# Optimization experiments

Hardware: AMD Instinct MI355X
Metric: run time of the kernel (lower is better)

The kernel has to match this reference:

```python
import jax, jax.numpy as jnp
import numpy as np

N = 50000       # num_nodes
E = 1_600_000   # num_edges (avg degree 32)
F_IN, HID, F_OUT = 128, 128, 64


def setup_inputs() -> dict:
    key = jax.random.key(0)
    k0, k1, k2, k3 = jax.random.split(key, 4)
    x = jax.random.normal(k0, (1, N, F_IN), dtype=jnp.float32)
    edge_index = jax.random.randint(k1, (2, E), 0, N, dtype=jnp.int32)
    # GCNConv weights (glorot-ish scale) and zero biases
    W1 = jax.random.normal(k2, (F_IN, HID), dtype=jnp.float32) / np.float32(np.sqrt(F_IN))
    b1 = jnp.zeros((HID,), dtype=jnp.float32)
    W2 = jax.random.normal(k3, (HID, F_OUT), dtype=jnp.float32) / np.float32(np.sqrt(HID))
    b2 = jnp.zeros((F_OUT,), dtype=jnp.float32)
    return {"x": x, "edge_index": edge_index, "W1": W1, "b1": b1, "W2": W2, "b2": b2}


def _gcn_layer(h, src, dst, norm, W, b, n):
    # linear transform then symmetric-normalized scatter-add aggregation
    h = h @ W                              # [N, F_out]
    msg = h[src] * norm[:, None]           # [E+N, F_out] gathered messages
    agg = jax.ops.segment_sum(msg, dst, num_segments=n)
    return agg + b


def reference(x, edge_index, W1, b1, W2, b2):
    xn = x[0]                              # [N, F_in] node feature matrix
    n = xn.shape[0]
    src, dst = edge_index[0], edge_index[1]
    # add self-loops (GCNConv default)
    loops = jnp.arange(n, dtype=src.dtype)
    src = jnp.concatenate([src, loops])
    dst = jnp.concatenate([dst, loops])
    # symmetric normalization: deg^-1/2[src] * deg^-1/2[dst] (deg >= 1 w/ self-loops)
    deg = jax.ops.segment_sum(jnp.ones(dst.shape, dtype=xn.dtype), dst, num_segments=n)
    dinv = jax.lax.rsqrt(deg)
    norm = dinv[src] * dinv[dst]
    h = jax.nn.relu(_gcn_layer(xn, src, dst, norm, W1, b1, n))
    out = jax.nn.relu(_gcn_layer(h, src, dst, norm, W2, b2, n))
    return out
```

## Files before the change

### kernel.cpp

```cpp
#include <hip/hip_runtime.h>
#include <hip/hip_fp16.h>


#define TILE 8192
#define BIN_CAP 2560

typedef _Float16 half8 __attribute__((ext_vector_type(8)));
typedef float floatx4 __attribute__((ext_vector_type(4)));

__global__ __launch_bounds__(256) void bin_kernel(const int* __restrict__ src,
                                                  const int* __restrict__ dst, int E,
                                                  int nbins,
                                                  int* __restrict__ binCnt,
                                                  unsigned* __restrict__ recs) {
    extern __shared__ int lds[];
    int* cnt = lds;
    int* gbase = lds + nbins;
    int tid = threadIdx.x;
    for (int i = tid; i < nbins; i += 256) cnt[i] = 0;
    __syncthreads();

    int t0 = blockIdx.x * TILE;
    int tEnd = min(t0 + TILE, E);

    for (int e = t0 + tid; e < tEnd; e += 256)
        atomicAdd(&cnt[dst[e] >> 6], 1);
    __syncthreads();

    for (int i = tid; i < nbins; i += 256) {
        int c = cnt[i];
        gbase[i] = (c > 0) ? atomicAdd(&binCnt[i], c) : 0;
        cnt[i] = 0;
    }
    __syncthreads();

    for (int e = t0 + tid; e < tEnd; e += 256) {
        int d = dst[e];
        int s = src[e];
        int b = d >> 6;
        int r = atomicAdd(&cnt[b], 1);
        int g = gbase[b] + r;
        if (g < BIN_CAP)
            recs[(size_t)b * BIN_CAP + g] = ((unsigned)(d & 63) << 16) | (unsigned)s;
    }
}

__global__ __launch_bounds__(256) void sort_bins(const unsigned* __restrict__ recs,
                                                 const int* __restrict__ binCnt,
                                                 unsigned short* __restrict__ sortedG,
                                                 int* __restrict__ startG,
                                                 float* __restrict__ dinv, int N) {
    __shared__ unsigned short sorted[BIN_CAP];
    __shared__ int c64[64];
    __shared__ int start[65];
    __shared__ int cursor[64];
    int b = blockIdx.x, tid = threadIdx.x;
    int lane = tid & 63, wave = tid >> 6;

    if (tid < 64) c64[tid] = 0;
    __syncthreads();
    int cnt = min(binCnt[b], BIN_CAP);
    const unsigned* bin = recs + (size_t)b * BIN_CAP;

    for (int i = tid; i < cnt; i += 256)
        atomicAdd(&c64[bin[i] >> 16], 1);
    __syncthreads();

    if (wave == 0) {
        int c = c64[lane];
        int v = c;
        #pragma unroll
        for (int off = 1; off < 64; off <<= 1) {
            int t = __shfl_up(v, off);
            if (lane >= off) v += t;
        }
        start[lane] = v - c;
        cursor[lane] = v - c;
        startG[b * 65 + lane] = v - c;
        if (lane == 63) { start[64] = v; startG[b * 65 + 64] = v; }
        int n = (b << 6) + lane;
        if (n < N) dinv[n] = rsqrtf((float)(c + 1));
    }
    __syncthreads();

    for (int i = tid; i < cnt; i += 256) {
        unsigned r = bin[i];
        int pos = atomicAdd(&cursor[r >> 16], 1);
        sorted[pos] = (unsigned short)(r & 0xFFFFu);
    }
    __syncthreads();
    unsigned short* sg = sortedG + (size_t)b * BIN_CAP;
    for (int i = tid; i < cnt; i += 256) sg[i] = sorted[i];
}

template <int COLS, bool FP32IN>
__global__ __launch_bounds__(256) void gemm_mfma(const void* __restrict__ Xv,
                                                 const float* __restrict__ W,
                                                 const float* __restrict__ dinv,
                                                 __half* __restrict__ Y, int N) {
    constexpr int LDA = 136;
    __shared__ __align__(16) _Float16 aT[64 * LDA];
    __shared__ __align__(16) _Float16 bT[COLS * LDA];

    int tid = threadIdx.x;
    int lane = tid & 63, wave = tid >> 6;
    int row0 = blockIdx.x * 64;

    for (int i = tid * 4; i < 64 * 128; i += 1024) {
        int r = i >> 7, k = i & 127;
        int gr = row0 + r;
        if (FP32IN) {
            float4 v = make_float4(0.f, 0.f, 0.f, 0.f);
            if (gr < N) v = *(const float4*)&((const float*)Xv)[(size_t)gr * 128 + k];
            __half2 p0 = __floats2half2_rn(v.x, v.y);
            __half2 p1 = __floats2half2_rn(v.z, v.w);
            *(uint2*)&aT[r * LDA + k] = make_uint2(*(uint*)&p0, *(uint*)&p1);
        } else {
            ushort4 u = make_ushort4(0, 0, 0, 0);
            if (gr < N) u = *(const ushort4*)&((const __half*)Xv)[(size_t)gr * 128 + k];
            *(ushort4*)&aT[r * LDA + k] = u;
        }
    }
    for (int i = tid; i < 128 * COLS; i += 256) {
        int k = i / COLS, n = i % COLS;
        bT[n * LDA + k] = (_Float16)W[i];
    }
    __syncthreads();

    constexpr int NT = COLS / 16;
    floatx4 acc[NT];
    #pragma unroll
    for (int t = 0; t < NT; t++) acc[t] = (floatx4){0.f, 0.f, 0.f, 0.f};

    int m = lane & 15, q = lane >> 4;
    const _Float16* arow = &aT[(wave * 16 + m) * LDA + q * 8];

    #pragma unroll
    for (int ks = 0; ks < 4; ks++) {
        half8 af = *(const half8*)&arow[ks * 32];
        #pragma unroll
        for (int t = 0; t < NT; t++) {
            half8 bf = *(const half8*)&bT[(t * 16 + m) * LDA + ks * 32 + q * 8];
            acc[t] = __builtin_amdgcn_mfma_f32_16x16x32_f16(af, bf, acc[t], 0, 0, 0);
        }
    }
    __syncthreads();

    float dv[4];
    #pragma unroll
    for (int r = 0; r < 4; r++) {
        int gr = row0 + wave * 16 + q * 4 + r;
        dv[r] = (gr < N) ? dinv[gr] : 0.0f;
    }
    #pragma unroll
    for (int t = 0; t < NT; t++)
        #pragma unroll
        for (int r = 0; r < 4; r++)
            aT[(wave * 16 + q * 4 + r) * LDA + t * 16 + m] = (_Float16)(dv[r] * acc[t][r]);
    __syncthreads();

    for (int i = tid; i < 64 * (COLS / 2); i += 256) {
        int r = i / (COLS / 2), c = i % (COLS / 2);
        int gr = row0 + r;
        if (gr < N)
            ((uint*)Y)[(size_t)gr * (COLS / 2) + c] = *(uint*)&aT[r * LDA + c * 2];
    }
}

__global__ __launch_bounds__(512) void agg_128(const __half* __restrict__ G,
                                               const unsigned short* __restrict__ sortedG,
                                               const int* __restrict__ startG,
                                               const float* __restrict__ dinv,
                                               const float* __restrict__ bias,
                                               __half* __restrict__ out, int N) {
    __shared__ unsigned short buf[BIN_CAP];
    __shared__ int st[33];
    int b = blockIdx.x, half_ = blockIdx.y;
    int tid = threadIdx.x, lane = tid & 63, wave = tid >> 6;
    int r0 = half_ * 32;

    if (tid < 33) st[tid] = startG[b * 65 + r0 + tid];
    __syncthreads();
    int S0 = st[0], S1 = st[32];
    const unsigned short* sg = sortedG + (size_t)b * BIN_CAP;
    for (int i = tid; i < S1 - S0; i += 512) buf[i] = sg[S0 + i];
    __syncthreads();

    float bx = bias[lane * 2], by = bias[lane * 2 + 1];
    for (int rr = 0; rr < 4; rr++) {
        int row = wave * 4 + rr;
        int n = (b << 6) + r0 + row;
        if (n >= N) continue;
        int jst = st[row] - S0, jen = st[row + 1] - S0;
        float2 self = __half22float2(*(const __half2*)&G[(size_t)n * 128 + lane * 2]);
        float ax = self.x, ay = self.y;
        int j = jst;
        for (; j + 8 <= jen; j += 8) {
            int s0 = buf[j],     s1 = buf[j + 1];
            int s2 = buf[j + 2], s3 = buf[j + 3];
            int s4 = buf[j + 4], s5 = buf[j + 5];
            int s6 = buf[j + 6], s7 = buf[j + 7];
            float2 v0 = __half22float2(*(const __half2*)&G[(size_t)s0 * 128 + lane * 2]);
            float2 v1 = __half22float2(*(const __half2*)&G[(size_t)s1 * 128 + lane * 2]);
            float2 v2 = __half22float2(*(const __half2*)&G[(size_t)s2 * 128 + lane * 2]);
            float2 v3 = __half22float2(*(const __half2*)&G[(size_t)s3 * 128 + lane * 2]);
            float2 v4 = __half22float2(*(const __half2*)&G[(size_t)s4 * 128 + lane * 2]);
            float2 v5 = __half22float2(*(const __half2*)&G[(size_t)s5 * 128 + lane * 2]);
            float2 v6 = __half22float2(*(const __half2*)&G[(size_t)s6 * 128 + lane * 2]);
            float2 v7 = __half22float2(*(const __half2*)&G[(size_t)s7 * 128 + lane * 2]);
            ax += ((v0.x + v1.x) + (v2.x + v3.x)) + ((v4.x + v5.x) + (v6.x + v7.x));
            ay += ((v0.y + v1.y) + (v2.y + v3.y)) + ((v4.y + v5.y) + (v6.y + v7.y));
        }
        for (; j < jen; j++) {
            int s = buf[j];
            float2 v = __half22float2(*(const __half2*)&G[(size_t)s * 128 + lane * 2]);
            ax += v.x; ay += v.y;
        }
        float di = dinv[n];
        float ox = fmaxf(fmaf(di, ax, bx), 0.0f);
        float oy = fmaxf(fmaf(di, ay, by), 0.0f);
        *(__half2*)&out[(size_t)n * 128 + lane * 2] = __floats2half2_rn(ox, oy);
    }
}

__global__ __launch_bounds__(512) void agg_64(const __half* __restrict__ G,
                                              const unsigned short* __restrict__ sortedG,
                                              const int* __restrict__ startG,
                                              const float* __restrict__ dinv,
                                              const float* __restrict__ bias,
                                              float* __restrict__ out, int N) {
    __shared__ unsigned short buf[BIN_CAP];
    __shared__ int st[33];
    int b = blockIdx.x, half_ = blockIdx.y;
    int tid = threadIdx.x, lane = tid & 63, wave = tid >> 6;
    int hl = lane & 31, side = lane >> 5;
    int r0 = half_ * 32;

    if (tid < 33) st[tid] = startG[b * 65 + r0 + tid];
    __syncthreads();
    int S0 = st[0], S1 = st[32];
    const unsigned short* sg = sortedG + (size_t)b * BIN_CAP;
    for (int i = tid; i < S1 - S0; i += 512) buf[i] = sg[S0 + i];
    __syncthreads();

    float bx = bias[hl * 2], by = bias[hl * 2 + 1];
    for (int pp = 0; pp < 2; pp++) {
        int row = wave * 4 + pp * 2 + side;
        int n = (b << 6) + r0 + row;
        bool live = (n < N);
        int jst = live ? (st[row] - S0) : 0;
        int jen = live ? (st[row + 1] - S0) : 0;
        float ax = 0.0f, ay = 0.0f;
        if (live) {
            float2 self = __half22float2(*(const __half2*)&G[(size_t)n * 64 + hl * 2]);
            ax = self.x; ay = self.y;
        }
        int j = jst;
        for (; j + 4 <= jen; j += 4) {
            int s0 = buf[j],     s1 = buf[j + 1];
            int s2 = buf[j + 2], s3 = buf[j + 3];
            float2 v0 = __half22float2(*(const __half2*)&G[(size_t)s0 * 64 + hl * 2]);
            float2 v1 = __half22float2(*(const __half2*)&G[(size_t)s1 * 64 + hl * 2]);
            float2 v2 = __half22float2(*(const __half2*)&G[(size_t)s2 * 64 + hl * 2]);
            float2 v3 = __half22float2(*(const __half2*)&G[(size_t)s3 * 64 + hl * 2]);
            ax += (v0.x + v1.x) + (v2.x + v3.x);
            ay += (v0.y + v1.y) + (v2.y + v3.y);
        }
        for (; j < jen; j++) {
            int s = buf[j];
            float2 v = __half22float2(*(const __half2*)&G[(size_t)s * 64 + hl * 2]);
            ax += v.x; ay += v.y;
        }
        if (live) {
            float di = dinv[n];
            float ox = fmaxf(fmaf(di, ax, bx), 0.0f);
            float oy = fmaxf(fmaf(di, ay, by), 0.0f);
            *(float2*)&out[(size_t)n * 64 + hl * 2] = make_float2(ox, oy);
        }
    }
}

extern "C" void kernel_launch(void* const* d_in, const int* in_sizes, int n_in,
                              void* d_out, int out_size, void* d_ws, size_t ws_size,
                              hipStream_t stream) {
    const float* x  = (const float*)d_in[0];
    const int*   ei = (const int*)d_in[1];
    const float* W1 = (const float*)d_in[2];
    const float* b1 = (const float*)d_in[3];
    const float* W2 = (const float*)d_in[4];
    const float* b2 = (const float*)d_in[5];
    float* out = (float*)d_out;

    const int HID  = in_sizes[3];
    const int F_IN = in_sizes[2] / HID;
    const int N    = in_sizes[0] / F_IN;
    const int E    = in_sizes[1] / 2;
    (void)n_in; (void)out_size; (void)ws_size; (void)F_IN;

    const int* src = ei;
    const int* dst = ei + E;

    const int nbins = (N + 63) >> 6;

    char* p = (char*)d_ws;
    auto carve = [&](size_t bytes) { void* q = (void*)p; p += (bytes + 255) & ~(size_t)255; return q; };
    int*            binCnt  = (int*)           carve((size_t)nbins * 4);
    float*          dinv    = (float*)         carve((size_t)N * 4);
    unsigned*       recs    = (unsigned*)      carve((size_t)nbins * BIN_CAP * 4);
    unsigned short* sortedG = (unsigned short*)carve((size_t)nbins * BIN_CAP * 2);
    int*            startG  = (int*)           carve((size_t)nbins * 65 * 4);
    __half*         bufG    = (__half*)        carve((size_t)N * 128 * 2);
    __half*         bufB    = (__half*)        carve((size_t)N * 128 * 2);

    hipMemsetAsync(binCnt, 0, (size_t)nbins * 4, stream);

    int numTiles = (E + TILE - 1) / TILE;
    size_t binLds = (size_t)nbins * 2 * 4;
    bin_kernel<<<numTiles, 256, binLds, stream>>>(src, dst, E, nbins, binCnt, recs);
    sort_bins<<<nbins, 256, 0, stream>>>(recs, binCnt, sortedG, startG, dinv, N);

    dim3 aggGrid(nbins, 2);
    int gemmGrid = (N + 63) / 64;

    gemm_mfma<128, true><<<gemmGrid, 256, 0, stream>>>(x, W1, dinv, bufG, N);
    agg_128<<<aggGrid, 512, 0, stream>>>(bufG, sortedG, startG, dinv, b1, bufB, N);

    gemm_mfma<64, false><<<gemmGrid, 256, 0, stream>>>(bufB, W2, dinv, bufG, N);
    agg_64<<<aggGrid, 512, 0, stream>>>(bufG, sortedG, startG, dinv, b2, out, N);
}
```

Before: 235.0 us.

## Vectorize neighbor gathers to 16-byte loads with multi-edge lane groups

The aggregation kernels now have each lane load 8 fp16 features (16 bytes) per neighbor instead of one half2. Each wave therefore processes 4 edges at once (128-wide layer) or 8 edges at once (64-wide layer), and the partial sums are merged with xor shuffles. The aim is fewer, wider gather instructions and more memory-level parallelism per wave, at the cost of extra shuffle reductions and more accumulator registers. Separately, the bin and sort kernels move from 256 to 512 threads per block.

```diff
diff --git a/kernel.cpp b/kernel.cpp
--- a/kernel.cpp
+++ b/kernel.cpp
@@ -8,7 +8,7 @@
 typedef _Float16 half8 __attribute__((ext_vector_type(8)));
 typedef float floatx4 __attribute__((ext_vector_type(4)));
 
-__global__ __launch_bounds__(256) void bin_kernel(const int* __restrict__ src,
+__global__ __launch_bounds__(512) void bin_kernel(const int* __restrict__ src,
                                                   const int* __restrict__ dst, int E,
                                                   int nbins,
                                                   int* __restrict__ binCnt,
@@ -17,24 +17,24 @@
     int* cnt = lds;
     int* gbase = lds + nbins;
     int tid = threadIdx.x;
-    for (int i = tid; i < nbins; i += 256) cnt[i] = 0;
+    for (int i = tid; i < nbins; i += 512) cnt[i] = 0;
     __syncthreads();
 
     int t0 = blockIdx.x * TILE;
     int tEnd = min(t0 + TILE, E);
 
-    for (int e = t0 + tid; e < tEnd; e += 256)
+    for (int e = t0 + tid; e < tEnd; e += 512)
         atomicAdd(&cnt[dst[e] >> 6], 1);
     __syncthreads();
 
-    for (int i = tid; i < nbins; i += 256) {
+    for (int i = tid; i < nbins; i += 512) {
         int c = cnt[i];
         gbase[i] = (c > 0) ? atomicAdd(&binCnt[i], c) : 0;
         cnt[i] = 0;
     }
     __syncthreads();
 
-    for (int e = t0 + tid; e < tEnd; e += 256) {
+    for (int e = t0 + tid; e < tEnd; e += 512) {
         int d = dst[e];
         int s = src[e];
         int b = d >> 6;
@@ -45,7 +45,7 @@
     }
 }
 
-__global__ __launch_bounds__(256) void sort_bins(const unsigned* __restrict__ recs,
+__global__ __launch_bounds__(512) void sort_bins(const unsigned* __restrict__ recs,
                                                  const int* __restrict__ binCnt,
                                                  unsigned short* __restrict__ sortedG,
                                                  int* __restrict__ startG,
@@ -62,7 +62,7 @@
     int cnt = min(binCnt[b], BIN_CAP);
     const unsigned* bin = recs + (size_t)b * BIN_CAP;
 
-    for (int i = tid; i < cnt; i += 256)
+    for (int i = tid; i < cnt; i += 512)
         atomicAdd(&c64[bin[i] >> 16], 1);
     __syncthreads();
 
@@ -83,14 +83,14 @@
     }
     __syncthreads();
 
-    for (int i = tid; i < cnt; i += 256) {
+    for (int i = tid; i < cnt; i += 512) {
         unsigned r = bin[i];
         int pos = atomicAdd(&cursor[r >> 16], 1);
         sorted[pos] = (unsigned short)(r & 0xFFFFu);
     }
     __syncthreads();
     unsigned short* sg = sortedG + (size_t)b * BIN_CAP;
-    for (int i = tid; i < cnt; i += 256) sg[i] = sorted[i];
+    for (int i = tid; i < cnt; i += 512) sg[i] = sorted[i];
 }
 
 template <int COLS, bool FP32IN>
@@ -177,6 +177,7 @@
     __shared__ int st[33];
     int b = blockIdx.x, half_ = blockIdx.y;
     int tid = threadIdx.x, lane = tid & 63, wave = tid >> 6;
+    int ql = lane & 15, quad = lane >> 4;
     int r0 = half_ * 32;
 
     if (tid < 33) st[tid] = startG[b * 65 + r0 + tid];
@@ -186,40 +187,66 @@
     for (int i = tid; i < S1 - S0; i += 512) buf[i] = sg[S0 + i];
     __syncthreads();
 
-    float bx = bias[lane * 2], by = bias[lane * 2 + 1];
+    float bb[8];
+    #pragma unroll
+    for (int k = 0; k < 4; k++) {
+        float2 t = *(const float2*)&bias[ql * 8 + k * 2];
+        bb[k * 2] = t.x; bb[k * 2 + 1] = t.y;
+    }
+
     for (int rr = 0; rr < 4; rr++) {
         int row = wave * 4 + rr;
         int n = (b << 6) + r0 + row;
         if (n >= N) continue;
         int jst = st[row] - S0, jen = st[row + 1] - S0;
-        float2 self = __half22float2(*(const __half2*)&G[(size_t)n * 128 + lane * 2]);
-        float ax = self.x, ay = self.y;
-        int j = jst;
-        for (; j + 8 <= jen; j += 8) {
-            int s0 = buf[j],     s1 = buf[j + 1];
-            int s2 = buf[j + 2], s3 = buf[j + 3];
-            int s4 = buf[j + 4], s5 = buf[j + 5];
-            int s6 = buf[j + 6], s7 = buf[j + 7];
-            float2 v0 = __half22float2(*(const __half2*)&G[(size_t)s0 * 128 + lane * 2]);
-            float2 v1 = __half22float2(*(const __half2*)&G[(size_t)s1 * 128 + lane * 2]);
-            float2 v2 = __half22float2(*(const __half2*)&G[(size_t)s2 * 128 + lane * 2]);
-            float2 v3 = __half22float2(*(const __half2*)&G[(size_t)s3 * 128 + lane * 2]);
-            float2 v4 = __half22float2(*(const __half2*)&G[(size_t)s4 * 128 + lane * 2]);
-            float2 v5 = __half22float2(*(const __half2*)&G[(size_t)s5 * 128 + lane * 2]);
-            float2 v6 = __half22float2(*(const __half2*)&G[(size_t)s6 * 128 + lane * 2]);
-            float2 v7 = __half22float2(*(const __half2*)&G[(size_t)s7 * 128 + lane * 2]);
-            ax += ((v0.x + v1.x) + (v2.x + v3.x)) + ((v4.x + v5.x) + (v6.x + v7.x));
-            ay += ((v0.y + v1.y) + (v2.y + v3.y)) + ((v4.y + v5.y) + (v6.y + v7.y));
-        }
-        for (; j < jen; j++) {
+
+        float ax[8] = {};
+        int j = jst + quad;
+        for (; j + 4 < jen; j += 8) {
+            int sA = buf[j], sB = buf[j + 4];
+            uint4 uA = *(const uint4*)&G[(size_t)sA * 128 + ql * 8];
+            uint4 uB = *(const uint4*)&G[(size_t)sB * 128 + ql * 8];
+            float2 f;
+            f = __half22float2(*(__half2*)&uA.x); ax[0] += f.x; ax[1] += f.y;
+            f = __half22float2(*(__half2*)&uA.y); ax[2] += f.x; ax[3] += f.y;
+            f = __half22float2(*(__half2*)&uA.z); ax[4] += f.x; ax[5] += f.y;
+            f = __half22float2(*(__half2*)&uA.w); ax[6] += f.x; ax[7] += f.y;
+            f = __half22float2(*(__half2*)&uB.x); ax[0] += f.x; ax[1] += f.y;
+            f = __half22float2(*(__half2*)&uB.y); ax[2] += f.x; ax[3] += f.y;
+            f = __half22float2(*(__half2*)&uB.z); ax[4] += f.x; ax[5] += f.y;
+            f = __half22float2(*(__half2*)&uB.w); ax[6] += f.x; ax[7] += f.y;
+        }
+        for (; j < jen; j += 4) {
             int s = buf[j];
-            float2 v = __half22float2(*(const __half2*)&G[(size_t)s * 128 + lane * 2]);
-            ax += v.x; ay += v.y;
-        }
-        float di = dinv[n];
-        float ox = fmaxf(fmaf(di, ax, bx), 0.0f);
-        float oy = fmaxf(fmaf(di, ay, by), 0.0f);
-        *(__half2*)&out[(size_t)n * 128 + lane * 2] = __floats2half2_rn(ox, oy);
+            uint4 u = *(const uint4*)&G[(size_t)s * 128 + ql * 8];
+            float2 f;
+            f = __half22float2(*(__half2*)&u.x); ax[0] += f.x; ax[1] += f.y;
+            f = __half22float2(*(__half2*)&u.y); ax[2] += f.x; ax[3] += f.y;
+            f = __half22float2(*(__half2*)&u.z); ax[4] += f.x; ax[5] += f.y;
+            f = __half22float2(*(__half2*)&u.w); ax[6] += f.x; ax[7] += f.y;
+        }
+        #pragma unroll
+        for (int k = 0; k < 8; k++) {
+            ax[k] += __shfl_xor(ax[k], 16);
+            ax[k] += __shfl_xor(ax[k], 32);
+        }
+        if (quad == 0) {
+            uint4 us = *(const uint4*)&G[(size_t)n * 128 + ql * 8];
+            float2 f;
+            f = __half22float2(*(__half2*)&us.x); ax[0] += f.x; ax[1] += f.y;
+            f = __half22float2(*(__half2*)&us.y); ax[2] += f.x; ax[3] += f.y;
+            f = __half22float2(*(__half2*)&us.z); ax[4] += f.x; ax[5] += f.y;
+            f = __half22float2(*(__half2*)&us.w); ax[6] += f.x; ax[7] += f.y;
+            float di = dinv[n];
+            __half2 h[4];
+            #pragma unroll
+            for (int k = 0; k < 4; k++) {
+                float o0 = fmaxf(fmaf(di, ax[k * 2],     bb[k * 2]),     0.0f);
+                float o1 = fmaxf(fmaf(di, ax[k * 2 + 1], bb[k * 2 + 1]), 0.0f);
+                h[k] = __floats2half2_rn(o0, o1);
+            }
+            *(uint4*)&out[(size_t)n * 128 + ql * 8] = *(uint4*)h;
+        }
     }
 }
 
@@ -233,7 +260,7 @@
     __shared__ int st[33];
     int b = blockIdx.x, half_ = blockIdx.y;
     int tid = threadIdx.x, lane = tid & 63, wave = tid >> 6;
-    int hl = lane & 31, side = lane >> 5;
+    int ol = lane & 7, oct = lane >> 3;
     int r0 = half_ * 32;
 
     if (tid < 33) st[tid] = startG[b * 65 + r0 + tid];
@@ -243,39 +270,66 @@
     for (int i = tid; i < S1 - S0; i += 512) buf[i] = sg[S0 + i];
     __syncthreads();
 
-    float bx = bias[hl * 2], by = bias[hl * 2 + 1];
-    for (int pp = 0; pp < 2; pp++) {
-        int row = wave * 4 + pp * 2 + side;
+    float bb[8];
+    #pragma unroll
+    for (int k = 0; k < 4; k++) {
+        float2 t = *(const float2*)&bias[ol * 8 + k * 2];
+        bb[k * 2] = t.x; bb[k * 2 + 1] = t.y;
+    }
+
+    for (int rr = 0; rr < 4; rr++) {
+        int row = wave * 4 + rr;
         int n = (b << 6) + r0 + row;
-        bool live = (n < N);
-        int jst = live ? (st[row] - S0) : 0;
-        int jen = live ? (st[row + 1] - S0) : 0;
-        float ax = 0.0f, ay = 0.0f;
-        if (live) {
-            float2 self = __half22float2(*(const __half2*)&G[(size_t)n * 64 + hl * 2]);
-            ax = self.x; ay = self.y;
-        }
-        int j = jst;
-        for (; j + 4 <= jen; j += 4) {
-            int s0 = buf[j],     s1 = buf[j + 1];
-            int s2 = buf[j + 2], s3 = buf[j + 3];
-            float2 v0 = __half22float2(*(const __half2*)&G[(size_t)s0 * 64 + hl * 2]);
-            float2 v1 = __half22float2(*(const __half2*)&G[(size_t)s1 * 64 + hl * 2]);
-            float2 v2 = __half22float2(*(const __half2*)&G[(size_t)s2 * 64 + hl * 2]);
-            float2 v3 = __half22float2(*(const __half2*)&G[(size_t)s3 * 64 + hl * 2]);
-            ax += (v0.x + v1.x) + (v2.x + v3.x);
-            ay += (v0.y + v1.y) + (v2.y + v3.y);
-        }
-        for (; j < jen; j++) {
+        if (n >= N) continue;
+        int jst = st[row] - S0, jen = st[row + 1] - S0;
+
+        float ax[8] = {};
+        int j = jst + oct;
+        for (; j + 8 < jen; j += 16) {
+            int sA = buf[j], sB = buf[j + 8];
+            uint4 uA = *(const uint4*)&G[(size_t)sA * 64 + ol * 8];
+            uint4 uB = *(const uint4*)&G[(size_t)sB * 64 + ol * 8];
+            float2 f;
+            f = __half22float2(*(__half2*)&uA.x); ax[0] += f.x; ax[1] += f.y;
+            f = __half22float2(*(__half2*)&uA.y); ax[2] += f.x; ax[3] += f.y;
+            f = __half22float2(*(__half2*)&uA.z); ax[4] += f.x; ax[5] += f.y;
+            f = __half22float2(*(__half2*)&uA.w); ax[6] += f.x; ax[7] += f.y;
+            f = __half22float2(*(__half2*)&uB.x); ax[0] += f.x; ax[1] += f.y;
+            f = __half22float2(*(__half2*)&uB.y); ax[2] += f.x; ax[3] += f.y;
+            f = __half22float2(*(__half2*)&uB.z); ax[4] += f.x; ax[5] += f.y;
+            f = __half22float2(*(__half2*)&uB.w); ax[6] += f.x; ax[7] += f.y;
+        }
+        for (; j < jen; j += 8) {
             int s = buf[j];
-            float2 v = __half22float2(*(const __half2*)&G[(size_t)s * 64 + hl * 2]);
-            ax += v.x; ay += v.y;
-        }
-        if (live) {
+            uint4 u = *(const uint4*)&G[(size_t)s * 64 + ol * 8];
+            float2 f;
+            f = __half22float2(*(__half2*)&u.x); ax[0] += f.x; ax[1] += f.y;
+            f = __half22float2(*(__half2*)&u.y); ax[2] += f.x; ax[3] += f.y;
+            f = __half22float2(*(__half2*)&u.z); ax[4] += f.x; ax[5] += f.y;
+            f = __half22float2(*(__half2*)&u.w); ax[6] += f.x; ax[7] += f.y;
+        }
+        #pragma unroll
+        for (int k = 0; k < 8; k++) {
+            ax[k] += __shfl_xor(ax[k], 8);
+            ax[k] += __shfl_xor(ax[k], 16);
+            ax[k] += __shfl_xor(ax[k], 32);
+        }
+        if (oct < 2) {
+            uint4 us = *(const uint4*)&G[(size_t)n * 64 + ol * 8];
+            float2 f;
+            f = __half22float2(*(__half2*)&us.x); ax[0] += f.x; ax[1] += f.y;
+            f = __half22float2(*(__half2*)&us.y); ax[2] += f.x; ax[3] += f.y;
+            f = __half22float2(*(__half2*)&us.z); ax[4] += f.x; ax[5] += f.y;
+            f = __half22float2(*(__half2*)&us.w); ax[6] += f.x; ax[7] += f.y;
             float di = dinv[n];
-            float ox = fmaxf(fmaf(di, ax, bx), 0.0f);
-            float oy = fmaxf(fmaf(di, ay, by), 0.0f);
-            *(float2*)&out[(size_t)n * 64 + hl * 2] = make_float2(ox, oy);
+            float o[8];
+            #pragma unroll
+            for (int k = 0; k < 8; k++)
+                o[k] = fmaxf(fmaf(di, ax[k], bb[k]), 0.0f);
+            if (oct == 0)
+                *(float4*)&out[(size_t)n * 64 + ol * 8] = make_float4(o[0], o[1], o[2], o[3]);
+            else
+                *(float4*)&out[(size_t)n * 64 + ol * 8 + 4] = make_float4(o[4], o[5], o[6], o[7]);
         }
     }
 }
@@ -316,8 +370,8 @@
 
     int numTiles = (E + TILE - 1) / TILE;
     size_t binLds = (size_t)nbins * 2 * 4;
-    bin_kernel<<<numTiles, 256, binLds, stream>>>(src, dst, E, nbins, binCnt, recs);
-    sort_bins<<<nbins, 256, 0, stream>>>(recs, binCnt, sortedG, startG, dinv, N);
+    bin_kernel<<<numTiles, 512, binLds, stream>>>(src, dst, E, nbins, binCnt, recs);
+    sort_bins<<<nbins, 512, 0, stream>>>(recs, binCnt, sortedG, startG, dinv, N);
 
     dim3 aggGrid(nbins, 2);
     int gemmGrid = (N + 63) / 64;
```

After: 218.2 us. -7.1%, faster.
